# Kernel tuning notes

Hardware: AMD Instinct MI355X
Metric: run time of the kernel (lower is better)

## Reference

```python
import jax, jax.numpy as jnp
import numpy as np

N_NODES = 50000
N_EDGES = 800000
D = 64


def setup_inputs() -> dict:
    key = jax.random.key(0)
    ks = jax.random.split(key, 8)
    scale = 1.0 / np.sqrt(D)
    x = jax.random.normal(ks[0], (N_NODES, D), dtype=jnp.float32)
    edge_index = jax.random.randint(ks[1], (2, N_EDGES), 0, N_NODES, dtype=jnp.int64)
    W1_root = jax.random.normal(ks[2], (D, D), dtype=jnp.float32) * scale
    W1_nbr = jax.random.normal(ks[3], (D, D), dtype=jnp.float32) * scale
    b1 = jnp.zeros((D,), dtype=jnp.float32)
    W2_root = jax.random.normal(ks[4], (D, D), dtype=jnp.float32) * scale
    W2_nbr = jax.random.normal(ks[5], (D, D), dtype=jnp.float32) * scale
    b2 = jnp.zeros((D,), dtype=jnp.float32)
    return {"x": x, "edge_index": edge_index,
            "W1_root": W1_root, "W1_nbr": W1_nbr, "b1": b1,
            "W2_root": W2_root, "W2_nbr": W2_nbr, "b2": b2}


def graph_conv(x, src, dst, W_root, W_nbr, b, n_nodes):
    # sum-aggregate neighbor features: msg j->i uses x[src], scattered to dst
    agg = jax.ops.segment_sum(x[src], dst, num_segments=n_nodes)  # [N, D]
    return x @ W_root + agg @ W_nbr + b


def reference(x, edge_index, W1_root, W1_nbr, b1, W2_root, W2_nbr, b2):
    src, dst = edge_index[0], edge_index[1]
    n = x.shape[0]
    h = jax.nn.relu(graph_conv(x, src, dst, W1_root, W1_nbr, b1, n))
    out = graph_conv(h, src, dst, W2_root, W2_nbr, b2, n)
    return out
```

## Files before the change

### kernel.cpp

```cpp
#include <hip/hip_runtime.h>

#define N_NODES 50000
#define N_EDGES 800000
#define D 64
#define NBUCKETS 782
#define NPB 64
#define BCAP 2048
#define SBLOCKS 256
#define CHUNK (N_EDGES / SBLOCKS)
#define MB ((N_NODES + 63) / 64)

typedef short bf16x8 __attribute__((ext_vector_type(8)));
typedef float f32x4  __attribute__((ext_vector_type(4)));

__device__ __forceinline__ unsigned short f2bf(float f) {
    unsigned u = __float_as_uint(f);
    return (unsigned short)((u + 0x7fffu + ((u >> 16) & 1u)) >> 16);
}
__device__ __forceinline__ float bflo(unsigned u) {
    return __uint_as_float(u << 16);
}
__device__ __forceinline__ float bfhi(unsigned u) {
    return __uint_as_float(u & 0xffff0000u);
}

__global__ void __launch_bounds__(256) prep_kernel(
    const float* __restrict__ W1r, const float* __restrict__ W1n,
    const float* __restrict__ W2r, const float* __restrict__ W2n,
    int* __restrict__ cursorPad, unsigned short* __restrict__ wt) {
    int t = threadIdx.x;
    if (blockIdx.x == 4) {
        for (int i = t; i < NBUCKETS * 16; i += 256) cursorPad[i] = 0;
        return;
    }
    const float* Wsrc = blockIdx.x == 0 ? W1r : blockIdx.x == 1 ? W1n
                      : blockIdx.x == 2 ? W2r : W2n;
    unsigned short* dstw = wt + blockIdx.x * D * D;
    for (int i = t; i < D * D; i += 256) {
        int k = i >> 6, c = i & 63;
        dstw[c * D + k] = f2bf(Wsrc[i]);
    }
}

__device__ __forceinline__ void scatter_body(
    const int* __restrict__ src, const int* __restrict__ dst,
    int* __restrict__ cursorPad, int* __restrict__ staged,
    char* smem, int bid, int t) {
    int* hist = (int*)smem;
    int* curs = (int*)(smem + 3200);
    int* pk   = (int*)(smem + 6400);
    unsigned short* bk = (unsigned short*)(smem + 6400 + 12500);
    for (int i = t; i < NBUCKETS; i += 256) hist[i] = 0;
    __syncthreads();
    int lo = bid * CHUNK;
    for (int i = t; i < CHUNK; i += 256) {
        int d = dst[lo + i];
        int s = src[lo + i];
        pk[i] = (s << 6) | (d & 63);
        bk[i] = (unsigned short)(d >> 6);
        atomicAdd(&hist[d >> 6], 1);
    }
    __syncthreads();
    for (int k = t; k < NBUCKETS; k += 256)
        if (hist[k] > 0)
            curs[k] = k * BCAP + atomicAdd(&cursorPad[k * 16], hist[k]);
    __syncthreads();
    for (int i = t; i < CHUNK; i += 256) {
        int b = bk[i];
        int pos = atomicAdd(&curs[b], 1);
        staged[pos] = pk[i];
    }
}

template<int XBF>
__device__ __forceinline__ void gemm_mfma_body(
    const float* __restrict__ Xf, const unsigned short* __restrict__ Xb,
    const unsigned short* __restrict__ Wtr, const unsigned short* __restrict__ Wtn,
    float* __restrict__ outR, unsigned short* __restrict__ outN,
    int node0, int tid) {
    int wave = tid >> 6, lane = tid & 63;
    int rbase = node0 + wave * 16;
    int rrow  = lane & 15;
    int kg    = lane >> 4;
    int row   = min(rbase + rrow, N_NODES - 1);

    bf16x8 a0, a1;
    if (XBF) {
        a0 = *(const bf16x8*)(Xb + (size_t)row * D + kg * 8);
        a1 = *(const bf16x8*)(Xb + (size_t)row * D + 32 + kg * 8);
    } else {
        const float* xp = Xf + (size_t)row * D + kg * 8;
#pragma unroll
        for (int j = 0; j < 8; j++) a0[j] = (short)f2bf(xp[j]);
#pragma unroll
        for (int j = 0; j < 8; j++) a1[j] = (short)f2bf(xp[32 + j]);
    }

    f32x4 accR[4], accN[4];
#pragma unroll
    for (int t = 0; t < 4; t++) {
        accR[t][0] = 0.f; accR[t][1] = 0.f; accR[t][2] = 0.f; accR[t][3] = 0.f;
        accN[t][0] = 0.f; accN[t][1] = 0.f; accN[t][2] = 0.f; accN[t][3] = 0.f;
    }

#pragma unroll
    for (int t = 0; t < 4; t++) {
        int c = t * 16 + rrow;
        bf16x8 br0 = *(const bf16x8*)(Wtr + c * D + kg * 8);
        bf16x8 br1 = *(const bf16x8*)(Wtr + c * D + 32 + kg * 8);
        bf16x8 bn0 = *(const bf16x8*)(Wtn + c * D + kg * 8);
        bf16x8 bn1 = *(const bf16x8*)(Wtn + c * D + 32 + kg * 8);
        accR[t] = __builtin_amdgcn_mfma_f32_16x16x32_bf16(a0, br0, accR[t], 0, 0, 0);
        accR[t] = __builtin_amdgcn_mfma_f32_16x16x32_bf16(a1, br1, accR[t], 0, 0, 0);
        accN[t] = __builtin_amdgcn_mfma_f32_16x16x32_bf16(a0, bn0, accN[t], 0, 0, 0);
        accN[t] = __builtin_amdgcn_mfma_f32_16x16x32_bf16(a1, bn1, accN[t], 0, 0, 0);
    }

#pragma unroll
    for (int t = 0; t < 4; t++) {
#pragma unroll
        for (int i = 0; i < 4; i++) {
            int n = rbase + kg * 4 + i;
            if (n < N_NODES) {
                int c = t * 16 + rrow;
                outR[(size_t)n * D + c] = accR[t][i];
                outN[(size_t)n * D + c] = f2bf(accN[t][i]);
            }
        }
    }
}

__global__ void __launch_bounds__(256) scatter_gemm1(
    const int* __restrict__ src, const int* __restrict__ dst,
    int* __restrict__ cursorPad, int* __restrict__ staged,
    const float* __restrict__ X, const unsigned short* __restrict__ wt,
    float* __restrict__ xr, unsigned short* __restrict__ xn) {
    __shared__ char smem[25600];
    if (blockIdx.x < SBLOCKS) {
        scatter_body(src, dst, cursorPad, staged, smem, blockIdx.x, threadIdx.x);
    } else {
        gemm_mfma_body<0>(X, (const unsigned short*)0,
                          wt + 0 * D * D, wt + 1 * D * D,
                          xr, xn, (blockIdx.x - SBLOCKS) * 64, threadIdx.x);
    }
}

__global__ void __launch_bounds__(256) csr_build_kernel(
    const int* __restrict__ cursorPad, const int* __restrict__ staged,
    int* __restrict__ csr, int* __restrict__ startEnd) {
    __shared__ int deg[NPB];
    __shared__ int sc[NPB];
    __shared__ int curs[NPB];
    __shared__ int lcsr[BCAP];
    int k = blockIdx.x;
    int t = threadIdx.x;
    int base = k * BCAP;
    int cnt  = cursorPad[k * 16];
    if (t < NPB) deg[t] = 0;
    __syncthreads();
    for (int i = t; i < cnt; i += 256)
        atomicAdd(&deg[staged[base + i] & 63], 1);
    __syncthreads();
    int v = (t < NPB) ? deg[t] : 0;
    if (t < NPB) sc[t] = v;
    __syncthreads();
#pragma unroll
    for (int d = 1; d < NPB; d <<= 1) {
        int u = (t < NPB && t >= d) ? sc[t - d] : 0;
        __syncthreads();
        if (t < NPB) sc[t] += u;
        __syncthreads();
    }
    if (t < NPB) {
        int start = sc[t] - v;
        int node = k * NPB + t;
        if (node < N_NODES) {
            int2 se; se.x = base + start; se.y = base + start + v;
            ((int2*)startEnd)[node] = se;
        }
        curs[t] = start;
    }
    __syncthreads();
    for (int i = t; i < cnt; i += 256) {
        int e = staged[base + i];
        int pos = atomicAdd(&curs[e & 63], 1);
        lcsr[pos] = e >> 6;
    }
    __syncthreads();
    for (int i = t; i < cnt; i += 256)
        csr[base + i] = lcsr[i];
}

__global__ void __launch_bounds__(512) gather1_gemm2(
    const unsigned short* __restrict__ Gsrc, const float* __restrict__ Root,
    const float* __restrict__ bias,
    const int* __restrict__ startEnd, const int* __restrict__ csr,
    const unsigned short* __restrict__ wt,
    float* __restrict__ hr, unsigned short* __restrict__ hn) {
    __shared__ unsigned short hlds[16][72];
    int tid = threadIdx.x;
    int wave = tid >> 6, lane = tid & 63;
    int n0 = blockIdx.x * 16;
    int nA = n0 + wave * 2;
    int nB = nA + 1;
    int sub = lane >> 3, fq = lane & 7;

    int4 se = *(const int4*)(startEnd + nA * 2);
    int jbA = se.x, jeA = se.y, jbB = se.z, jeB = se.w;

    float4 xA0, xA1, xB0, xB1, b0, b1;
    if (sub == 0) {
        const float* rpA = Root + (size_t)nA * D + fq * 8;
        const float* rpB = Root + (size_t)nB * D + fq * 8;
        xA0 = *(const float4*)rpA; xA1 = *(const float4*)(rpA + 4);
        xB0 = *(const float4*)rpB; xB1 = *(const float4*)(rpB + 4);
        b0 = ((const float4*)bias)[fq * 2];
        b1 = ((const float4*)bias)[fq * 2 + 1];
    }

    float aA0=0.f,aA1=0.f,aA2=0.f,aA3=0.f,aA4=0.f,aA5=0.f,aA6=0.f,aA7=0.f;
    float aB0=0.f,aB1=0.f,aB2=0.f,aB3=0.f,aB4=0.f,aB5=0.f,aB6=0.f,aB7=0.f;

    while (jbA < jeA || jbB < jeB) {
        int pA = 0, pB = 0, mA = 0, mB = 0;
        if (jbA < jeA) {
            int idx = jbA + lane;
            pA = csr[idx < jeA ? idx : (jeA - 1)];
            mA = min(64, jeA - jbA);
        }
        if (jbB < jeB) {
            int idx = jbB + lane;
            pB = csr[idx < jeB ? idx : (jeB - 1)];
            mB = min(64, jeB - jbB);
        }
        if (mA) {
            int b = 0;
            for (; b + 16 <= mA; b += 16) {
                int i0 = __shfl(pA, b + sub, 64);
                int i1 = __shfl(pA, b + 8 + sub, 64);
                uint4 u0 = *(const uint4*)(Gsrc + i0 * D + fq * 8);
                uint4 u1 = *(const uint4*)(Gsrc + i1 * D + fq * 8);
                aA0 += bflo(u0.x) + bflo(u1.x);  aA1 += bfhi(u0.x) + bfhi(u1.x);
                aA2 += bflo(u0.y) + bflo(u1.y);  aA3 += bfhi(u0.y) + bfhi(u1.y);
                aA4 += bflo(u0.z) + bflo(u1.z);  aA5 += bfhi(u0.z) + bfhi(u1.z);
                aA6 += bflo(u0.w) + bflo(u1.w);  aA7 += bfhi(u0.w) + bfhi(u1.w);
            }
            for (; b < mA; b += 8) {
                int sidx = b + sub;
                int scl = sidx < mA ? sidx : (mA - 1);
                int i0 = __shfl(pA, scl, 64);
                if (sidx < mA) {
                    uint4 u = *(const uint4*)(Gsrc + i0 * D + fq * 8);
                    aA0 += bflo(u.x); aA1 += bfhi(u.x);
                    aA2 += bflo(u.y); aA3 += bfhi(u.y);
                    aA4 += bflo(u.z); aA5 += bfhi(u.z);
                    aA6 += bflo(u.w); aA7 += bfhi(u.w);
                }
            }
        }
        if (mB) {
            int b = 0;
            for (; b + 16 <= mB; b += 16) {
                int i0 = __shfl(pB, b + sub, 64);
                int i1 = __shfl(pB, b + 8 + sub, 64);
                uint4 u0 = *(const uint4*)(Gsrc + i0 * D + fq * 8);
                uint4 u1 = *(const uint4*)(Gsrc + i1 * D + fq * 8);
                aB0 += bflo(u0.x) + bflo(u1.x);  aB1 += bfhi(u0.x) + bfhi(u1.x);
                aB2 += bflo(u0.y) + bflo(u1.y);  aB3 += bfhi(u0.y) + bfhi(u1.y);
                aB4 += bflo(u0.z) + bflo(u1.z);  aB5 += bfhi(u0.z) + bfhi(u1.z);
                aB6 += bflo(u0.w) + bflo(u1.w);  aB7 += bfhi(u0.w) + bfhi(u1.w);
            }
            for (; b < mB; b += 8) {
                int sidx = b + sub;
                int scl = sidx < mB ? sidx : (mB - 1);
                int i0 = __shfl(pB, scl, 64);
                if (sidx < mB) {
                    uint4 u = *(const uint4*)(Gsrc + i0 * D + fq * 8);
                    aB0 += bflo(u.x); aB1 += bfhi(u.x);
                    aB2 += bflo(u.y); aB3 += bfhi(u.y);
                    aB4 += bflo(u.z); aB5 += bfhi(u.z);
                    aB6 += bflo(u.w); aB7 += bfhi(u.w);
                }
            }
        }
        jbA += 64; jbB += 64;
    }

#pragma unroll
    for (int mk = 8; mk <= 32; mk <<= 1) {
        aA0 += __shfl_xor(aA0, mk, 64); aA1 += __shfl_xor(aA1, mk, 64);
        aA2 += __shfl_xor(aA2, mk, 64); aA3 += __shfl_xor(aA3, mk, 64);
        aA4 += __shfl_xor(aA4, mk, 64); aA5 += __shfl_xor(aA5, mk, 64);
        aA6 += __shfl_xor(aA6, mk, 64); aA7 += __shfl_xor(aA7, mk, 64);
        aB0 += __shfl_xor(aB0, mk, 64); aB1 += __shfl_xor(aB1, mk, 64);
        aB2 += __shfl_xor(aB2, mk, 64); aB3 += __shfl_xor(aB3, mk, 64);
        aB4 += __shfl_xor(aB4, mk, 64); aB5 += __shfl_xor(aB5, mk, 64);
        aB6 += __shfl_xor(aB6, mk, 64); aB7 += __shfl_xor(aB7, mk, 64);
    }
    if (sub == 0) {
        float r0 = fmaxf(aA0 + xA0.x + b0.x, 0.f), r1 = fmaxf(aA1 + xA0.y + b0.y, 0.f);
        float r2 = fmaxf(aA2 + xA0.z + b0.z, 0.f), r3 = fmaxf(aA3 + xA0.w + b0.w, 0.f);
        float r4 = fmaxf(aA4 + xA1.x + b1.x, 0.f), r5 = fmaxf(aA5 + xA1.y + b1.y, 0.f);
        float r6 = fmaxf(aA6 + xA1.z + b1.z, 0.f), r7 = fmaxf(aA7 + xA1.w + b1.w, 0.f);
        float s0 = fmaxf(aB0 + xB0.x + b0.x, 0.f), s1 = fmaxf(aB1 + xB0.y + b0.y, 0.f);
        float s2 = fmaxf(aB2 + xB0.z + b0.z, 0.f), s3 = fmaxf(aB3 + xB0.w + b0.w, 0.f);
        float s4 = fmaxf(aB4 + xB1.x + b1.x, 0.f), s5 = fmaxf(aB5 + xB1.y + b1.y, 0.f);
        float s6 = fmaxf(aB6 + xB1.z + b1.z, 0.f), s7 = fmaxf(aB7 + xB1.w + b1.w, 0.f);
        uint4 u;
        u.x = (unsigned)f2bf(r0) | ((unsigned)f2bf(r1) << 16);
        u.y = (unsigned)f2bf(r2) | ((unsigned)f2bf(r3) << 16);
        u.z = (unsigned)f2bf(r4) | ((unsigned)f2bf(r5) << 16);
        u.w = (unsigned)f2bf(r6) | ((unsigned)f2bf(r7) << 16);
        *(uint4*)&hlds[wave * 2][fq * 8] = u;
        u.x = (unsigned)f2bf(s0) | ((unsigned)f2bf(s1) << 16);
        u.y = (unsigned)f2bf(s2) | ((unsigned)f2bf(s3) << 16);
        u.z = (unsigned)f2bf(s4) | ((unsigned)f2bf(s5) << 16);
        u.w = (unsigned)f2bf(s6) | ((unsigned)f2bf(s7) << 16);
        *(uint4*)&hlds[wave * 2 + 1][fq * 8] = u;
    }
    __syncthreads();

    int t4   = wave >> 1;
    int kind = wave & 1;
    int rrow = lane & 15;
    int kg   = lane >> 4;
    bf16x8 a0 = *(const bf16x8*)&hlds[rrow][kg * 8];
    bf16x8 a1 = *(const bf16x8*)&hlds[rrow][32 + kg * 8];
    const unsigned short* Wt = wt + (2 + kind) * D * D;
    int c = t4 * 16 + rrow;
    bf16x8 bw0 = *(const bf16x8*)(Wt + c * D + kg * 8);
    bf16x8 bw1 = *(const bf16x8*)(Wt + c * D + 32 + kg * 8);
    f32x4 acc;
    acc[0] = 0.f; acc[1] = 0.f; acc[2] = 0.f; acc[3] = 0.f;
    acc = __builtin_amdgcn_mfma_f32_16x16x32_bf16(a0, bw0, acc, 0, 0, 0);
    acc = __builtin_amdgcn_mfma_f32_16x16x32_bf16(a1, bw1, acc, 0, 0, 0);
    if (kind == 0) {
#pragma unroll
        for (int i = 0; i < 4; i++)
            hr[(size_t)(n0 + kg * 4 + i) * D + c] = acc[i];
    } else {
#pragma unroll
        for (int i = 0; i < 4; i++)
            hn[(size_t)(n0 + kg * 4 + i) * D + c] = f2bf(acc[i]);
    }
}

__global__ void __launch_bounds__(256) gather2_out(
    const unsigned short* __restrict__ Gsrc, const float* __restrict__ Root,
    const float* __restrict__ bias,
    const int* __restrict__ startEnd, const int* __restrict__ csr,
    float* __restrict__ outF) {
    int tid = threadIdx.x;
    int wave = tid >> 6, lane = tid & 63;
    int nA = blockIdx.x * 8 + wave * 2;
    int nB = nA + 1;
    int sub = lane >> 3, fq = lane & 7;

    int4 se = *(const int4*)(startEnd + nA * 2);
    int jbA = se.x, jeA = se.y, jbB = se.z, jeB = se.w;

    float4 xA0, xA1, xB0, xB1, b0, b1;
    if (sub == 0) {
        const float* rpA = Root + (size_t)nA * D + fq * 8;
        const float* rpB = Root + (size_t)nB * D + fq * 8;
        xA0 = *(const float4*)rpA; xA1 = *(const float4*)(rpA + 4);
        xB0 = *(const float4*)rpB; xB1 = *(const float4*)(rpB + 4);
        b0 = ((const float4*)bias)[fq * 2];
        b1 = ((const float4*)bias)[fq * 2 + 1];
    }

    float aA0=0.f,aA1=0.f,aA2=0.f,aA3=0.f,aA4=0.f,aA5=0.f,aA6=0.f,aA7=0.f;
    float aB0=0.f,aB1=0.f,aB2=0.f,aB3=0.f,aB4=0.f,aB5=0.f,aB6=0.f,aB7=0.f;

    while (jbA < jeA || jbB < jeB) {
        int pA = 0, pB = 0, mA = 0, mB = 0;
        if (jbA < jeA) {
            int idx = jbA + lane;
            pA = csr[idx < jeA ? idx : (jeA - 1)];
            mA = min(64, jeA - jbA);
        }
        if (jbB < jeB) {
            int idx = jbB + lane;
            pB = csr[idx < jeB ? idx : (jeB - 1)];
            mB = min(64, jeB - jbB);
        }
        if (mA) {
            int b = 0;
            for (; b + 16 <= mA; b += 16) {
                int i0 = __shfl(pA, b + sub, 64);
                int i1 = __shfl(pA, b + 8 + sub, 64);
                uint4 u0 = *(const uint4*)(Gsrc + i0 * D + fq * 8);
                uint4 u1 = *(const uint4*)(Gsrc + i1 * D + fq * 8);
                aA0 += bflo(u0.x) + bflo(u1.x);  aA1 += bfhi(u0.x) + bfhi(u1.x);
                aA2 += bflo(u0.y) + bflo(u1.y);  aA3 += bfhi(u0.y) + bfhi(u1.y);
                aA4 += bflo(u0.z) + bflo(u1.z);  aA5 += bfhi(u0.z) + bfhi(u1.z);
                aA6 += bflo(u0.w) + bflo(u1.w);  aA7 += bfhi(u0.w) + bfhi(u1.w);
            }
            for (; b < mA; b += 8) {
                int sidx = b + sub;
                int scl = sidx < mA ? sidx : (mA - 1);
                int i0 = __shfl(pA, scl, 64);
                if (sidx < mA) {
                    uint4 u = *(const uint4*)(Gsrc + i0 * D + fq * 8);
                    aA0 += bflo(u.x); aA1 += bfhi(u.x);
                    aA2 += bflo(u.y); aA3 += bfhi(u.y);
                    aA4 += bflo(u.z); aA5 += bfhi(u.z);
                    aA6 += bflo(u.w); aA7 += bfhi(u.w);
                }
            }
        }
        if (mB) {
            int b = 0;
            for (; b + 16 <= mB; b += 16) {
                int i0 = __shfl(pB, b + sub, 64);
                int i1 = __shfl(pB, b + 8 + sub, 64);
                uint4 u0 = *(const uint4*)(Gsrc + i0 * D + fq * 8);
                uint4 u1 = *(const uint4*)(Gsrc + i1 * D + fq * 8);
                aB0 += bflo(u0.x) + bflo(u1.x);  aB1 += bfhi(u0.x) + bfhi(u1.x);
                aB2 += bflo(u0.y) + bflo(u1.y);  aB3 += bfhi(u0.y) + bfhi(u1.y);
                aB4 += bflo(u0.z) + bflo(u1.z);  aB5 += bfhi(u0.z) + bfhi(u1.z);
                aB6 += bflo(u0.w) + bflo(u1.w);  aB7 += bfhi(u0.w) + bfhi(u1.w);
            }
            for (; b < mB; b += 8) {
                int sidx = b + sub;
                int scl = sidx < mB ? sidx : (mB - 1);
                int i0 = __shfl(pB, scl, 64);
                if (sidx < mB) {
                    uint4 u = *(const uint4*)(Gsrc + i0 * D + fq * 8);
                    aB0 += bflo(u.x); aB1 += bfhi(u.x);
                    aB2 += bflo(u.y); aB3 += bfhi(u.y);
                    aB4 += bflo(u.z); aB5 += bfhi(u.z);
                    aB6 += bflo(u.w); aB7 += bfhi(u.w);
                }
            }
        }
        jbA += 64; jbB += 64;
    }

#pragma unroll
    for (int mk = 8; mk <= 32; mk <<= 1) {
        aA0 += __shfl_xor(aA0, mk, 64); aA1 += __shfl_xor(aA1, mk, 64);
        aA2 += __shfl_xor(aA2, mk, 64); aA3 += __shfl_xor(aA3, mk, 64);
        aA4 += __shfl_xor(aA4, mk, 64); aA5 += __shfl_xor(aA5, mk, 64);
        aA6 += __shfl_xor(aA6, mk, 64); aA7 += __shfl_xor(aA7, mk, 64);
        aB0 += __shfl_xor(aB0, mk, 64); aB1 += __shfl_xor(aB1, mk, 64);
        aB2 += __shfl_xor(aB2, mk, 64); aB3 += __shfl_xor(aB3, mk, 64);
        aB4 += __shfl_xor(aB4, mk, 64); aB5 += __shfl_xor(aB5, mk, 64);
        aB6 += __shfl_xor(aB6, mk, 64); aB7 += __shfl_xor(aB7, mk, 64);
    }
    if (sub == 0) {
        float4 w0, w1;
        w0.x = aA0 + xA0.x + b0.x; w0.y = aA1 + xA0.y + b0.y;
        w0.z = aA2 + xA0.z + b0.z; w0.w = aA3 + xA0.w + b0.w;
        w1.x = aA4 + xA1.x + b1.x; w1.y = aA5 + xA1.y + b1.y;
        w1.z = aA6 + xA1.z + b1.z; w1.w = aA7 + xA1.w + b1.w;
        *(float4*)(outF + (size_t)nA * D + fq * 8) = w0;
        *(float4*)(outF + (size_t)nA * D + fq * 8 + 4) = w1;
        w0.x = aB0 + xB0.x + b0.x; w0.y = aB1 + xB0.y + b0.y;
        w0.z = aB2 + xB0.z + b0.z; w0.w = aB3 + xB0.w + b0.w;
        w1.x = aB4 + xB1.x + b1.x; w1.y = aB5 + xB1.y + b1.y;
        w1.z = aB6 + xB1.z + b1.z; w1.w = aB7 + xB1.w + b1.w;
        *(float4*)(outF + (size_t)nB * D + fq * 8) = w0;
        *(float4*)(outF + (size_t)nB * D + fq * 8 + 4) = w1;
    }
}

extern "C" void kernel_launch(void* const* d_in, const int* in_sizes, int n_in,
                              void* d_out, int out_size, void* d_ws, size_t ws_size,
                              hipStream_t stream) {
    const float* x   = (const float*)d_in[0];
    const int*   edg = (const int*)d_in[1];
    const float* W1r = (const float*)d_in[2];
    const float* W1n = (const float*)d_in[3];
    const float* b1  = (const float*)d_in[4];
    const float* W2r = (const float*)d_in[5];
    const float* W2n = (const float*)d_in[6];
    const float* b2  = (const float*)d_in[7];
    float* out = (float*)d_out;

    const int* src = edg;
    const int* dst = edg + N_EDGES;

    int* W              = (int*)d_ws;
    int* cursorPad      = W;
    int* staged         = W + NBUCKETS * 16;
    int* csr            = staged + NBUCKETS * BCAP;
    int* startEnd       = csr + NBUCKETS * BCAP;
    float* xr           = (float*)(startEnd + 2 * N_NODES);
    unsigned short* xn  = (unsigned short*)(xr + (size_t)N_NODES * D);
    float* hr           = (float*)(xn + (size_t)N_NODES * D);
    unsigned short* hn  = (unsigned short*)(hr + (size_t)N_NODES * D);
    unsigned short* wt  = hn + (size_t)N_NODES * D;

    prep_kernel<<<5, 256, 0, stream>>>(W1r, W1n, W2r, W2n, cursorPad, wt);

    scatter_gemm1<<<SBLOCKS + MB, 256, 0, stream>>>(
        src, dst, cursorPad, staged, x, wt, xr, xn);

    csr_build_kernel<<<NBUCKETS, 256, 0, stream>>>(cursorPad, staged, csr,
                                                   startEnd);

    gather1_gemm2<<<N_NODES / 16, 512, 0, stream>>>(
        xn, xr, b1, startEnd, csr, wt, hr, hn);

    gather2_out<<<N_NODES / 8, 256, 0, stream>>>(
        hn, hr, b2, startEnd, csr, out);
}
```

Before: 168.3 us.

## Fuse CSR build into layer-1 gather kernel with 16-node buckets

Shrinks destination buckets from 64 to 16 nodes so that one bucket maps to one 16-node gather block. The CSR-build kernel is folded into gather1_gemm2: each block sorts its bucket's staged edges in LDS, writes csr/startEnd for the second layer, and gathers from the LDS copy instead of global memory. This removes one kernel launch and a global round trip for the first-layer adjacency. In exchange the scatter needs more LDS for its histograms, there are more cursor atomics, and BCAP 512 leaves less headroom against bucket overflow.

```diff
diff --git a/kernel.cpp b/kernel.cpp
--- a/kernel.cpp
+++ b/kernel.cpp
@@ -3,9 +3,9 @@
 #define N_NODES 50000
 #define N_EDGES 800000
 #define D 64
-#define NBUCKETS 782
-#define NPB 64
-#define BCAP 2048
+#define NBUCKETS 3125
+#define NPB 16
+#define BCAP 512
 #define SBLOCKS 256
 #define CHUNK (N_EDGES / SBLOCKS)
 #define MB ((N_NODES + 63) / 64)
@@ -29,8 +29,10 @@
     const float* __restrict__ W2r, const float* __restrict__ W2n,
     int* __restrict__ cursorPad, unsigned short* __restrict__ wt) {
     int t = threadIdx.x;
-    if (blockIdx.x == 4) {
-        for (int i = t; i < NBUCKETS * 16; i += 256) cursorPad[i] = 0;
+    if (blockIdx.x >= 4) {
+        int lo = (blockIdx.x - 4) * (NBUCKETS * 16 / 8);
+        int hi = lo + (NBUCKETS * 16 / 8);
+        for (int i = lo + t; i < hi; i += 256) cursorPad[i] = 0;
         return;
     }
     const float* Wsrc = blockIdx.x == 0 ? W1r : blockIdx.x == 1 ? W1n
@@ -47,18 +49,18 @@
     int* __restrict__ cursorPad, int* __restrict__ staged,
     char* smem, int bid, int t) {
     int* hist = (int*)smem;
-    int* curs = (int*)(smem + 3200);
-    int* pk   = (int*)(smem + 6400);
-    unsigned short* bk = (unsigned short*)(smem + 6400 + 12500);
+    int* curs = (int*)(smem + 12500);
+    int* pk   = (int*)(smem + 25000);
+    unsigned short* bk = (unsigned short*)(smem + 37500);
     for (int i = t; i < NBUCKETS; i += 256) hist[i] = 0;
     __syncthreads();
     int lo = bid * CHUNK;
     for (int i = t; i < CHUNK; i += 256) {
         int d = dst[lo + i];
         int s = src[lo + i];
-        pk[i] = (s << 6) | (d & 63);
-        bk[i] = (unsigned short)(d >> 6);
-        atomicAdd(&hist[d >> 6], 1);
+        pk[i] = (s << 4) | (d & 15);
+        bk[i] = (unsigned short)(d >> 4);
+        atomicAdd(&hist[d >> 4], 1);
     }
     __syncthreads();
     for (int k = t; k < NBUCKETS; k += 256)
@@ -135,7 +137,7 @@
     int* __restrict__ cursorPad, int* __restrict__ staged,
     const float* __restrict__ X, const unsigned short* __restrict__ wt,
     float* __restrict__ xr, unsigned short* __restrict__ xn) {
-    __shared__ char smem[25600];
+    __shared__ char smem[43776];
     if (blockIdx.x < SBLOCKS) {
         scatter_body(src, dst, cursorPad, staged, smem, blockIdx.x, threadIdx.x);
     } else {
@@ -145,68 +147,52 @@
     }
 }
 
-__global__ void __launch_bounds__(256) csr_build_kernel(
+__global__ void __launch_bounds__(512) gather1_gemm2(
     const int* __restrict__ cursorPad, const int* __restrict__ staged,
-    int* __restrict__ csr, int* __restrict__ startEnd) {
-    __shared__ int deg[NPB];
-    __shared__ int sc[NPB];
-    __shared__ int curs[NPB];
+    int* __restrict__ csr, int* __restrict__ startEnd,
+    const unsigned short* __restrict__ Gsrc, const float* __restrict__ Root,
+    const float* __restrict__ bias, const unsigned short* __restrict__ wt,
+    float* __restrict__ hr, unsigned short* __restrict__ hn) {
+    __shared__ int sdeg[NPB];
+    __shared__ int sstart[NPB];
+    __shared__ int scurs[NPB];
     __shared__ int lcsr[BCAP];
+    __shared__ unsigned short hlds[16][72];
     int k = blockIdx.x;
-    int t = threadIdx.x;
-    int base = k * BCAP;
-    int cnt  = cursorPad[k * 16];
-    if (t < NPB) deg[t] = 0;
-    __syncthreads();
-    for (int i = t; i < cnt; i += 256)
-        atomicAdd(&deg[staged[base + i] & 63], 1);
-    __syncthreads();
-    int v = (t < NPB) ? deg[t] : 0;
-    if (t < NPB) sc[t] = v;
-    __syncthreads();
-#pragma unroll
-    for (int d = 1; d < NPB; d <<= 1) {
-        int u = (t < NPB && t >= d) ? sc[t - d] : 0;
-        __syncthreads();
-        if (t < NPB) sc[t] += u;
-        __syncthreads();
-    }
-    if (t < NPB) {
-        int start = sc[t] - v;
-        int node = k * NPB + t;
-        if (node < N_NODES) {
-            int2 se; se.x = base + start; se.y = base + start + v;
-            ((int2*)startEnd)[node] = se;
-        }
-        curs[t] = start;
-    }
-    __syncthreads();
-    for (int i = t; i < cnt; i += 256) {
-        int e = staged[base + i];
-        int pos = atomicAdd(&curs[e & 63], 1);
-        lcsr[pos] = e >> 6;
-    }
-    __syncthreads();
-    for (int i = t; i < cnt; i += 256)
-        csr[base + i] = lcsr[i];
-}
-
-__global__ void __launch_bounds__(512) gather1_gemm2(
-    const unsigned short* __restrict__ Gsrc, const float* __restrict__ Root,
-    const float* __restrict__ bias,
-    const int* __restrict__ startEnd, const int* __restrict__ csr,
-    const unsigned short* __restrict__ wt,
-    float* __restrict__ hr, unsigned short* __restrict__ hn) {
-    __shared__ unsigned short hlds[16][72];
     int tid = threadIdx.x;
+    int gbase = k * BCAP;
+    int cnt = cursorPad[k * 16];
+
+    if (tid < NPB) sdeg[tid] = 0;
+    __syncthreads();
+    for (int i = tid; i < cnt; i += 512)
+        atomicAdd(&sdeg[staged[gbase + i] & 15], 1);
+    __syncthreads();
+    if (tid == 0) {
+        int acc = 0;
+#pragma unroll
+        for (int j = 0; j < NPB; j++) { sstart[j] = acc; scurs[j] = acc; acc += sdeg[j]; }
+    }
+    __syncthreads();
+    for (int i = tid; i < cnt; i += 512) {
+        int e = staged[gbase + i];
+        int pos = atomicAdd(&scurs[e & 15], 1);
+        lcsr[pos] = e >> 4;
+    }
+    __syncthreads();
+    for (int i = tid; i < cnt; i += 512) csr[gbase + i] = lcsr[i];
+    if (tid < NPB) {
+        int2 se; se.x = gbase + sstart[tid]; se.y = gbase + sstart[tid] + sdeg[tid];
+        ((int2*)startEnd)[k * NPB + tid] = se;
+    }
+
     int wave = tid >> 6, lane = tid & 63;
-    int n0 = blockIdx.x * 16;
-    int nA = n0 + wave * 2;
-    int nB = nA + 1;
+    int cA = wave * 2, cB = cA + 1;
+    int n0 = k * NPB;
+    int nA = n0 + cA, nB = n0 + cB;
     int sub = lane >> 3, fq = lane & 7;
-
-    int4 se = *(const int4*)(startEnd + nA * 2);
-    int jbA = se.x, jeA = se.y, jbB = se.z, jeB = se.w;
+    int jbA = sstart[cA], jeA = jbA + sdeg[cA];
+    int jbB = sstart[cB], jeB = jbB + sdeg[cB];
 
     float4 xA0, xA1, xB0, xB1, b0, b1;
     if (sub == 0) {
@@ -225,12 +211,12 @@
         int pA = 0, pB = 0, mA = 0, mB = 0;
         if (jbA < jeA) {
             int idx = jbA + lane;
-            pA = csr[idx < jeA ? idx : (jeA - 1)];
+            pA = lcsr[idx < jeA ? idx : (jeA - 1)];
             mA = min(64, jeA - jbA);
         }
         if (jbB < jeB) {
             int idx = jbB + lane;
-            pB = csr[idx < jeB ? idx : (jeB - 1)];
+            pB = lcsr[idx < jeB ? idx : (jeB - 1)];
             mB = min(64, jeB - jbB);
         }
         if (mA) {
@@ -311,12 +297,12 @@
         u.y = (unsigned)f2bf(r2) | ((unsigned)f2bf(r3) << 16);
         u.z = (unsigned)f2bf(r4) | ((unsigned)f2bf(r5) << 16);
         u.w = (unsigned)f2bf(r6) | ((unsigned)f2bf(r7) << 16);
-        *(uint4*)&hlds[wave * 2][fq * 8] = u;
+        *(uint4*)&hlds[cA][fq * 8] = u;
         u.x = (unsigned)f2bf(s0) | ((unsigned)f2bf(s1) << 16);
         u.y = (unsigned)f2bf(s2) | ((unsigned)f2bf(s3) << 16);
         u.z = (unsigned)f2bf(s4) | ((unsigned)f2bf(s5) << 16);
         u.w = (unsigned)f2bf(s6) | ((unsigned)f2bf(s7) << 16);
-        *(uint4*)&hlds[wave * 2 + 1][fq * 8] = u;
+        *(uint4*)&hlds[cB][fq * 8] = u;
     }
     __syncthreads();
 
@@ -492,16 +478,13 @@
     unsigned short* hn  = (unsigned short*)(hr + (size_t)N_NODES * D);
     unsigned short* wt  = hn + (size_t)N_NODES * D;
 
-    prep_kernel<<<5, 256, 0, stream>>>(W1r, W1n, W2r, W2n, cursorPad, wt);
+    prep_kernel<<<12, 256, 0, stream>>>(W1r, W1n, W2r, W2n, cursorPad, wt);
 
     scatter_gemm1<<<SBLOCKS + MB, 256, 0, stream>>>(
         src, dst, cursorPad, staged, x, wt, xr, xn);
 
-    csr_build_kernel<<<NBUCKETS, 256, 0, stream>>>(cursorPad, staged, csr,
-                                                   startEnd);
-
-    gather1_gemm2<<<N_NODES / 16, 512, 0, stream>>>(
-        xn, xr, b1, startEnd, csr, wt, hr, hn);
+    gather1_gemm2<<<NBUCKETS, 512, 0, stream>>>(
+        cursorPad, staged, csr, startEnd, xn, xr, b1, wt, hr, hn);
 
     gather2_out<<<N_NODES / 8, 256, 0, stream>>>(
         hn, hr, b2, startEnd, csr, out);
```

Measured after the change: 187.4 us. 11.3% more time.
